# Kernel tuning notes

Hardware: AMD Instinct MI355X
Metric: run time of the kernel (lower is better)

Reference implementation:

```python
import jax, jax.numpy as jnp
import numpy as np

D, H, K = 384, 6, 8

def _ln(x, g, b, eps=1e-5):
    mu = jnp.mean(x, axis=-1, keepdims=True)
    var = jnp.mean((x - mu) ** 2, axis=-1, keepdims=True)
    return (x - mu) * jax.lax.rsqrt(var + eps) * g + b

def setup_inputs() -> dict:
    key = jax.random.key(0)
    ks = jax.random.split(key, 20)
    B, N = 4, 2048
    s = 0.02
    inp = {
        'x': jax.random.normal(ks[0], (B, N, D), jnp.float32),
        'knn_index': jax.random.randint(ks[1], (B * K * N,), 0, B * N, jnp.int64),
        'ln1_g': jnp.ones((D,), jnp.float32),
        'ln1_b': jnp.zeros((D,), jnp.float32),
        'w_qkv': jax.random.normal(ks[2], (D, 3 * D), jnp.float32) * s,
        'w_proj': jax.random.normal(ks[3], (D, D), jnp.float32) * s,
        'b_proj': jnp.zeros((D,), jnp.float32),
        'w_knn': jax.random.normal(ks[4], (2 * D, D), jnp.float32) * s,
        'b_knn': jnp.zeros((D,), jnp.float32),
        'w_g1': jax.random.normal(ks[5], (2 * D, D), jnp.float32) * s,
        'b_g1': jnp.zeros((D,), jnp.float32),
        'w_g2': jax.random.normal(ks[6], (D, D), jnp.float32) * s,
        'b_g2': jnp.zeros((D,), jnp.float32),
        'ln2_g': jnp.ones((D,), jnp.float32),
        'ln2_b': jnp.zeros((D,), jnp.float32),
        'w_fc1': jax.random.normal(ks[7], (D, 4 * D), jnp.float32) * s,
        'b_fc1': jnp.zeros((4 * D,), jnp.float32),
        'w_fc2': jax.random.normal(ks[8], (4 * D, D), jnp.float32) * s,
        'b_fc2': jnp.zeros((D,), jnp.float32),
    }
    return inp

def reference(x, knn_index, ln1_g, ln1_b, w_qkv, w_proj, b_proj, w_knn, b_knn,
              w_g1, b_g1, w_g2, b_g2, ln2_g, ln2_b, w_fc1, b_fc1, w_fc2, b_fc2):
    B, N, _ = x.shape
    hd = D // H
    scale = hd ** -0.5
    nx = _ln(x, ln1_g, ln1_b)
    # --- self attention ---
    qkv = (nx @ w_qkv).reshape(B, N, 3, H, hd).transpose(2, 0, 3, 1, 4)  # [3,B,H,N,hd]
    q, k, v = qkv[0], qkv[1], qkv[2]
    attn = jax.nn.softmax(jnp.einsum('bhnd,bhmd->bhnm', q * scale, k), axis=-1)
    attn_out = jnp.einsum('bhnm,bhmd->bhnd', attn, v).transpose(0, 2, 1, 3).reshape(B, N, D)
    attn_out = attn_out @ w_proj + b_proj
    # --- EdgeConv-style graph feature: gather-concat-MLP-maxpool ---
    feat = nx.reshape(B * N, D)[knn_index].reshape(B, K, N, D)
    xe = jnp.broadcast_to(nx[:, None], (B, K, N, D))
    gf = jnp.concatenate([feat - xe, xe], axis=-1)  # [B,K,N,2D]
    knn_out = jnp.max(jax.nn.leaky_relu(gf @ w_knn + b_knn, 0.2), axis=1)  # [B,N,D]
    # --- salience gate ---
    gi = jnp.concatenate([attn_out, knn_out], axis=-1)
    gate = jax.nn.sigmoid(jax.nn.gelu(gi @ w_g1 + b_g1, approximate=False) @ w_g2 + b_g2)
    fused = (1 - gate) * attn_out + gate * knn_out
    x = x + fused
    # --- FFN ---
    h = jax.nn.gelu(_ln(x, ln2_g, ln2_b) @ w_fc1 + b_fc1, approximate=False)
    x = x + (h @ w_fc2 + b_fc2)
    return x
```

## Files before the change

kernel.cpp:

```cpp
#include <hip/hip_runtime.h>
#include <math.h>

typedef unsigned short u16;
typedef __attribute__((ext_vector_type(8))) short short8;
typedef __attribute__((ext_vector_type(4))) float floatx4;
typedef __attribute__((ext_vector_type(4))) short sh4v;

union sh4u { sh4v v; u16 u[4]; };
union sh8u { short8 v; u16 u[8]; };

__device__ __forceinline__ floatx4 mfma16(short8 a, short8 b, floatx4 c) {
  return __builtin_amdgcn_mfma_f32_16x16x32_bf16(a, b, c, 0, 0, 0);
}

__device__ __forceinline__ floatx4 zero4() {
  floatx4 z = {0.f, 0.f, 0.f, 0.f};
  return z;
}

__device__ __forceinline__ u16 f2b(float f) {
  union { float f; unsigned u; } v; v.f = f;
  unsigned u = v.u;
  return (u16)((u + 0x7FFFu + ((u >> 16) & 1u)) >> 16);
}

__device__ __forceinline__ float b2f(u16 u) {
  union { unsigned u; float f; } v; v.u = ((unsigned)u) << 16;
  return v.f;
}

__device__ __forceinline__ float gelu_exact(float x) {
  return 0.5f * x * (1.f + erff(x * 0.70710678118654752440f));
}

__device__ __forceinline__ unsigned pack2(float a, float b) {
  return (unsigned)f2b(a) | ((unsigned)f2b(b) << 16);
}

__device__ __forceinline__ unsigned permpack(float p0, float p1) {
  return __builtin_amdgcn_perm(__float_as_uint(p1), __float_as_uint(p0), 0x07060302u);
}

__global__ __launch_bounds__(256) void tcln_kernel(
    const float* __restrict__ p0, const float* __restrict__ p1,
    const float* __restrict__ p2, const float* __restrict__ p3,
    const float* __restrict__ p4, const float* __restrict__ p5,
    const float* __restrict__ wknn,
    u16* __restrict__ o0, u16* __restrict__ o1, u16* __restrict__ o2,
    u16* __restrict__ o3, u16* __restrict__ o4, u16* __restrict__ o5,
    u16* __restrict__ wcT,
    const float* __restrict__ x, const float* __restrict__ g,
    const float* __restrict__ bia, u16* __restrict__ nx) {
  __shared__ u16 L[64][66];
  int t = blockIdx.x, tid = threadIdx.x;
  if (t >= 612) {
    int wave = tid >> 6, lane = tid & 63;
    int row = (t - 612) * 4 + wave;
    const float* xr = x + (size_t)row * 384;
    float v[6];
    float s = 0.f;
#pragma unroll
    for (int j = 0; j < 6; j++) { v[j] = xr[lane + 64 * j]; s += v[j]; }
#pragma unroll
    for (int off = 32; off > 0; off >>= 1) s += __shfl_xor(s, off);
    float mu = s * (1.f / 384.f);
    float ss = 0.f;
#pragma unroll
    for (int j = 0; j < 6; j++) { float d = v[j] - mu; ss += d * d; }
#pragma unroll
    for (int off = 32; off > 0; off >>= 1) ss += __shfl_xor(ss, off);
    float rstd = rsqrtf(ss * (1.f / 384.f) + 1e-5f);
    u16* orow = nx + (size_t)row * 384;
#pragma unroll
    for (int j = 0; j < 6; j++) {
      int d = lane + 64 * j;
      orow[d] = f2b((v[j] - mu) * rstd * g[d] + bia[d]);
    }
    return;
  }
  if (t >= 540) {
    t -= 540;
    int tk = t / 12, tn = t % 12;
    int k0 = tk * 64, j0 = tn * 64;
#pragma unroll
    for (int i = 0; i < 4; i++) {
      int c = tid + 256 * i;
      int r = c >> 4, c4 = (c & 15) * 4;
      floatx4 v;
      if (j0 < 384) {
        v = *(const floatx4*)(wknn + (size_t)(k0 + r) * 384 + j0 + c4);
      } else {
        floatx4 a = *(const floatx4*)(wknn + (size_t)(384 + k0 + r) * 384 + (j0 - 384) + c4);
        floatx4 b = *(const floatx4*)(wknn + (size_t)(k0 + r) * 384 + (j0 - 384) + c4);
        v = a - b;
      }
      *(unsigned*)&L[r][c4]     = pack2(v[0], v[1]);
      *(unsigned*)&L[r][c4 + 2] = pack2(v[2], v[3]);
    }
    __syncthreads();
#pragma unroll
    for (int i = 0; i < 2; i++) {
      int c = tid + 256 * i;
      int nn = c >> 3, k8 = (c & 7) * 8;
      sh8u pk;
#pragma unroll
      for (int j = 0; j < 8; j++) pk.u[j] = L[k8 + j][nn];
      *(short8*)(wcT + (size_t)(j0 + nn) * 384 + k0 + k8) = pk.v;
    }
    return;
  }
  const float* src; u16* dst; int Kd, Nd, tk, tn;
  if      (t < 108) { src = p0; dst = o0; Kd = 384;  Nd = 1152; tk = t / 18; tn = t % 18; }
  else if (t < 144) { src = p1; dst = o1; Kd = 384;  Nd = 384;  t -= 108; tk = t / 6;  tn = t % 6; }
  else if (t < 216) { src = p2; dst = o2; Kd = 768;  Nd = 384;  t -= 144; tk = t / 6;  tn = t % 6; }
  else if (t < 252) { src = p3; dst = o3; Kd = 384;  Nd = 384;  t -= 216; tk = t / 6;  tn = t % 6; }
  else if (t < 396) { src = p4; dst = o4; Kd = 384;  Nd = 1536; t -= 252; tk = t / 24; tn = t % 24; }
  else              { src = p5; dst = o5; Kd = 1536; Nd = 384;  t -= 396; tk = t / 6;  tn = t % 6; }
  int k0 = tk * 64, n0 = tn * 64;
#pragma unroll
  for (int i = 0; i < 4; i++) {
    int c = tid + 256 * i;
    int r = c >> 4, c4 = (c & 15) * 4;
    floatx4 v = *(const floatx4*)(src + (size_t)(k0 + r) * Nd + n0 + c4);
    *(unsigned*)&L[r][c4]     = pack2(v[0], v[1]);
    *(unsigned*)&L[r][c4 + 2] = pack2(v[2], v[3]);
  }
  __syncthreads();
#pragma unroll
  for (int i = 0; i < 2; i++) {
    int c = tid + 256 * i;
    int nn = c >> 3, k8 = (c & 7) * 8;
    sh8u pk;
#pragma unroll
    for (int j = 0; j < 8; j++) pk.u[j] = L[k8 + j][nn];
    *(short8*)(dst + (size_t)(n0 + nn) * Kd + k0 + k8) = pk.v;
  }
}

__global__ __launch_bounds__(256) void lnb_kernel(const u16* __restrict__ x,
                                                  const float* __restrict__ g,
                                                  const float* __restrict__ bia,
                                                  u16* __restrict__ out) {
  int wave = threadIdx.x >> 6, lane = threadIdx.x & 63;
  int row = blockIdx.x * 4 + wave;
  const u16* xr = x + (size_t)row * 384;
  float v[6];
  float s = 0.f;
#pragma unroll
  for (int j = 0; j < 6; j++) { v[j] = b2f(xr[lane + 64 * j]); s += v[j]; }
#pragma unroll
  for (int off = 32; off > 0; off >>= 1) s += __shfl_xor(s, off);
  float mu = s * (1.f / 384.f);
  float ss = 0.f;
#pragma unroll
  for (int j = 0; j < 6; j++) { float d = v[j] - mu; ss += d * d; }
#pragma unroll
  for (int off = 32; off > 0; off >>= 1) ss += __shfl_xor(ss, off);
  float rstd = rsqrtf(ss * (1.f / 384.f) + 1e-5f);
  u16* orow = out + (size_t)row * 384;
#pragma unroll
  for (int j = 0; j < 6; j++) {
    int d = lane + 64 * j;
    orow[d] = f2b((v[j] - mu) * rstd * g[d] + bia[d]);
  }
}

template <int EPI>
__global__ __launch_bounds__(256) void gemm128_kernel(
    const u16* __restrict__ A0, const u16* __restrict__ A1, int Ksplit,
    const u16* __restrict__ BwT, const u16* __restrict__ BwT2, int N, int K,
    const float* __restrict__ bias,
    float* __restrict__ outF, u16* __restrict__ outB, u16* __restrict__ outB2,
    const u16* __restrict__ eA16, const u16* __restrict__ eK16,
    const float* __restrict__ eX, u16* __restrict__ outV) {
  __shared__ u16 As[128][72];
  __shared__ u16 Bs[128][72];
  int tid = threadIdx.x;
  int lane = tid & 63, wave = tid >> 6, quad = lane >> 4, l16 = lane & 15;
  int n0 = blockIdx.x * 128, m0 = blockIdx.y * 128;
  int wm = (wave >> 1) * 64, wn = (wave & 1) * 64;
  const u16* Bsrc = BwT;
  int nbase = n0;
  if (EPI == 8 && n0 >= 1152) { Bsrc = BwT2; nbase = n0 - 1152; }
  floatx4 acc[4][4];
#pragma unroll
  for (int i = 0; i < 4; i++)
#pragma unroll
    for (int j = 0; j < 4; j++) acc[i][j] = zero4();

  for (int k0 = 0; k0 < K; k0 += 64) {
    const u16* Ap;
    int kk, sA;
    if (k0 < Ksplit) { Ap = A0; kk = k0; sA = Ksplit; }
    else             { Ap = A1; kk = k0 - Ksplit; sA = K - Ksplit; }
#pragma unroll
    for (int i = 0; i < 4; i++) {
      int c = tid + 256 * i;
      int row = c >> 3, c8 = (c & 7) * 8;
      *(short8*)&As[row][c8] =
          *(const short8*)(Ap + (size_t)(m0 + row) * sA + kk + c8);
      *(short8*)&Bs[row][c8] =
          *(const short8*)(Bsrc + (size_t)(nbase + row) * K + k0 + c8);
    }
    __syncthreads();
#pragma unroll
    for (int kh = 0; kh < 2; kh++) {
      short8 af[4], bfr[4];
#pragma unroll
      for (int ti = 0; ti < 4; ti++)
        af[ti] = *(const short8*)&As[wm + ti * 16 + l16][kh * 32 + quad * 8];
#pragma unroll
      for (int tj = 0; tj < 4; tj++)
        bfr[tj] = *(const short8*)&Bs[wn + tj * 16 + l16][kh * 32 + quad * 8];
#pragma unroll
      for (int ti = 0; ti < 4; ti++)
#pragma unroll
        for (int tj = 0; tj < 4; tj++)
          acc[ti][tj] = mfma16(af[ti], bfr[tj], acc[ti][tj]);
    }
    __syncthreads();
  }

#pragma unroll
  for (int ti = 0; ti < 4; ti++)
#pragma unroll
    for (int tj = 0; tj < 4; tj++) {
      int col = n0 + wn + tj * 16 + l16;
      int row0 = m0 + wm + ti * 16 + quad * 4;
      if (EPI == 8) {
        if (n0 < 1152) {
          float sc = (col < 384) ? 0.18033688011112042f : 1.f;
          sh4u pk;
#pragma unroll
          for (int r = 0; r < 4; r++) {
            u16 bv = f2b(acc[ti][tj][r] * sc);
            outB[(size_t)(row0 + r) * 1152 + col] = bv;
            pk.u[r] = bv;
          }
          if (col >= 768) {
            int b = row0 >> 11, n = row0 & 2047;
            int hd = col - 768;
            *(sh4v*)(outV + ((size_t)(b * 6 + (hd >> 6)) * 64 + (hd & 63)) * 2048 + n) = pk.v;
          }
        } else {
#pragma unroll
          for (int r = 0; r < 4; r++)
            outB2[(size_t)(row0 + r) * 768 + (col - 1152)] = f2b(acc[ti][tj][r]);
        }
      } else {
#pragma unroll
        for (int r = 0; r < 4; r++) {
          size_t rc = (size_t)(row0 + r) * N + col;
          float v = acc[ti][tj][r];
          if (EPI == 3) {
            outB[rc] = f2b(gelu_exact(v + bias[col]));
          } else if (EPI == 4) {
            float gte = 1.f / (1.f + __expf(-(v + bias[col])));
            float fu = (1.f - gte) * b2f(eA16[rc]) + gte * b2f(eK16[rc]);
            outB[rc] = f2b(eX[rc] + fu);
          } else if (EPI == 7) {
            outF[rc] = v + bias[col] + b2f(eA16[rc]);
          }
        }
      }
    }
}

__global__ __launch_bounds__(256) void attn1_kernel(const u16* __restrict__ qkv,
                                                    const u16* __restrict__ Vt,
                                                    u16* __restrict__ OPb,
                                                    float* __restrict__ LS) {
  __shared__ u16 Ks[64][72];
  __shared__ u16 Vts[64][72];
  __shared__ u16 Ps[4][32][72];
  int tid = threadIdx.x;
  int lane = tid & 63, w = tid >> 6, quad = lane >> 4, l16 = lane & 15;
  int bh = blockIdx.y, b = bh / 6, h = bh % 6;
  int q0 = blockIdx.x * 128, split = blockIdx.z;
  const u16* qbase = qkv + (size_t)b * 2048 * 1152 + h * 64;
  const u16* kbase = qbase + 384 + (size_t)split * 512 * 1152;
  const u16* vtb = Vt + (size_t)bh * 64 * 2048 + split * 512;
  short8 qf[2][2];
#pragma unroll
  for (int s = 0; s < 2; s++) {
    int qrow = q0 + w * 32 + s * 16 + l16;
    qf[s][0] = *(const short8*)(qbase + (size_t)qrow * 1152 + quad * 8);
    qf[s][1] = *(const short8*)(qbase + (size_t)qrow * 1152 + 32 + quad * 8);
  }
  floatx4 O[4][2];
  float lsum[2] = {0.f, 0.f};
#pragma unroll
  for (int i = 0; i < 4; i++)
#pragma unroll
    for (int s = 0; s < 2; s++) O[i][s] = zero4();

  int rb = tid >> 3, c8 = (tid & 7) * 8;
  short8 rk[2], rv[2];
  rk[0] = *(const short8*)(kbase + (size_t)rb * 1152 + c8);
  rk[1] = *(const short8*)(kbase + (size_t)(rb + 32) * 1152 + c8);
  rv[0] = *(const short8*)(vtb + (size_t)rb * 2048 + c8);
  rv[1] = *(const short8*)(vtb + (size_t)(rb + 32) * 2048 + c8);

  for (int kt = 0; kt < 8; kt++) {
    __syncthreads();
    *(short8*)&Ks[rb][c8] = rk[0];
    *(short8*)&Ks[rb + 32][c8] = rk[1];
    *(short8*)&Vts[rb][c8] = rv[0];
    *(short8*)&Vts[rb + 32][c8] = rv[1];
    __syncthreads();
    if (kt < 7) {
      int key0 = (kt + 1) * 64;
      rk[0] = *(const short8*)(kbase + (size_t)(key0 + rb) * 1152 + c8);
      rk[1] = *(const short8*)(kbase + (size_t)(key0 + rb + 32) * 1152 + c8);
      rv[0] = *(const short8*)(vtb + (size_t)rb * 2048 + key0 + c8);
      rv[1] = *(const short8*)(vtb + (size_t)(rb + 32) * 2048 + key0 + c8);
    }
#pragma unroll
    for (int mt = 0; mt < 4; mt++) {
      short8 k0 = *(const short8*)&Ks[mt * 16 + l16][quad * 8];
      short8 k1 = *(const short8*)&Ks[mt * 16 + l16][32 + quad * 8];
#pragma unroll
      for (int s = 0; s < 2; s++) {
        floatx4 st = mfma16(k0, qf[s][0], zero4());
        st = mfma16(k1, qf[s][1], st);
        float p0 = exp2f(st[0]), p1 = exp2f(st[1]);
        float p2 = exp2f(st[2]), p3 = exp2f(st[3]);
        lsum[s] += (p0 + p1) + (p2 + p3);
        uint2 pk;
        pk.x = permpack(p0, p1);
        pk.y = permpack(p2, p3);
        *(uint2*)&Ps[w][s * 16 + l16][mt * 16 + quad * 4] = pk;
      }
    }
    short8 pf[2][2];
#pragma unroll
    for (int s = 0; s < 2; s++) {
      pf[s][0] = *(const short8*)&Ps[w][s * 16 + l16][quad * 8];
      pf[s][1] = *(const short8*)&Ps[w][s * 16 + l16][32 + quad * 8];
    }
#pragma unroll
    for (int mt2 = 0; mt2 < 4; mt2++) {
      short8 v0 = *(const short8*)&Vts[mt2 * 16 + l16][quad * 8];
      short8 v1 = *(const short8*)&Vts[mt2 * 16 + l16][32 + quad * 8];
#pragma unroll
      for (int s = 0; s < 2; s++) {
        O[mt2][s] = mfma16(v0, pf[s][0], O[mt2][s]);
        O[mt2][s] = mfma16(v1, pf[s][1], O[mt2][s]);
      }
    }
  }
#pragma unroll
  for (int s = 0; s < 2; s++) {
    lsum[s] += __shfl_xor(lsum[s], 16);
    lsum[s] += __shfl_xor(lsum[s], 32);
    int row = b * 2048 + q0 + w * 32 + s * 16 + l16;
    u16* orow = OPb + (size_t)split * 8192 * 384 + (size_t)row * 384 + h * 64;
#pragma unroll
    for (int mt2 = 0; mt2 < 4; mt2++) {
      sh4u pk;
#pragma unroll
      for (int r = 0; r < 4; r++) pk.u[r] = f2b(O[mt2][s][r]);
      *(sh4v*)(orow + mt2 * 16 + quad * 4) = pk.v;
    }
    if (quad == 0) LS[split * 8192 + row] = lsum[s];
  }
}

__global__ __launch_bounds__(256) void projknn_kernel(
    const u16* __restrict__ OPb, const float* __restrict__ LS,
    const u16* __restrict__ BwT, const float* __restrict__ bias,
    u16* __restrict__ outB,
    const u16* __restrict__ GBb, const int* __restrict__ kidx,
    const float* __restrict__ bknn, u16* __restrict__ knn_bf) {
  __shared__ u16 As[128][72];
  __shared__ u16 Bs[128][72];
  int bid = blockIdx.x, tid = threadIdx.x;
  if (bid >= 192) {
    int wave = tid >> 6, lane = tid & 63;
    int row = (bid - 192) * 4 + wave;
    int b = row >> 11, n = row & 2047;
    float base[6], acc[6];
#pragma unroll
    for (int j = 0; j < 6; j++) {
      int d = lane + 64 * j;
      base[j] = b2f(GBb[(size_t)row * 768 + 384 + d]) + bknn[d];
      acc[j] = -1e30f;
    }
    for (int kk = 0; kk < 8; kk++) {
      int g = kidx[(b * 8 + kk) * 2048 + n];
      const u16* Gr = GBb + (size_t)g * 768;
#pragma unroll
      for (int j = 0; j < 6; j++) {
        float v = b2f(Gr[lane + 64 * j]) + base[j];
        v = v > 0.f ? v : 0.2f * v;
        acc[j] = fmaxf(acc[j], v);
      }
    }
#pragma unroll
    for (int j = 0; j < 6; j++)
      knn_bf[(size_t)row * 384 + lane + 64 * j] = f2b(acc[j]);
    return;
  }
  int lane = tid & 63, wave = tid >> 6, quad = lane >> 4, l16 = lane & 15;
  int n0 = (bid % 3) * 128, m0 = (bid / 3) * 128;
  int wm = (wave >> 1) * 64, wn = (wave & 1) * 64;
  floatx4 acc[4][4];
#pragma unroll
  for (int i = 0; i < 4; i++)
#pragma unroll
    for (int j = 0; j < 4; j++) acc[i][j] = zero4();

  const size_t SP = (size_t)8192 * 384;
  for (int k0 = 0; k0 < 384; k0 += 64) {
#pragma unroll
    for (int i = 0; i < 4; i++) {
      int c = tid + 256 * i;
      int row = c >> 3, c8 = (c & 7) * 8;
      int gr = m0 + row;
      float rl = 1.f / ((LS[gr] + LS[8192 + gr]) + (LS[16384 + gr] + LS[24576 + gr]));
      const u16* p0 = OPb + (size_t)gr * 384 + k0 + c8;
      sh8u a0, a1, a2, a3, pk;
      a0.v = *(const short8*)p0;
      a1.v = *(const short8*)(p0 + SP);
      a2.v = *(const short8*)(p0 + 2 * SP);
      a3.v = *(const short8*)(p0 + 3 * SP);
#pragma unroll
      for (int j = 0; j < 8; j++)
        pk.u[j] = f2b(((b2f(a0.u[j]) + b2f(a1.u[j])) + (b2f(a2.u[j]) + b2f(a3.u[j]))) * rl);
      *(short8*)&As[row][c8] = pk.v;
      *(short8*)&Bs[row][c8] =
          *(const short8*)(BwT + (size_t)(n0 + row) * 384 + k0 + c8);
    }
    __syncthreads();
#pragma unroll
    for (int kh = 0; kh < 2; kh++) {
      short8 af[4], bfr[4];
#pragma unroll
      for (int ti = 0; ti < 4; ti++)
        af[ti] = *(const short8*)&As[wm + ti * 16 + l16][kh * 32 + quad * 8];
#pragma unroll
      for (int tj = 0; tj < 4; tj++)
        bfr[tj] = *(const short8*)&Bs[wn + tj * 16 + l16][kh * 32 + quad * 8];
#pragma unroll
      for (int ti = 0; ti < 4; ti++)
#pragma unroll
        for (int tj = 0; tj < 4; tj++)
          acc[ti][tj] = mfma16(af[ti], bfr[tj], acc[ti][tj]);
    }
    __syncthreads();
  }
#pragma unroll
  for (int ti = 0; ti < 4; ti++)
#pragma unroll
    for (int tj = 0; tj < 4; tj++) {
      int col = n0 + wn + tj * 16 + l16;
      int row0 = m0 + wm + ti * 16 + quad * 4;
#pragma unroll
      for (int r = 0; r < 4; r++)
        outB[(size_t)(row0 + r) * 384 + col] = f2b(acc[ti][tj][r] + bias[col]);
    }
}

extern "C" void kernel_launch(void* const* d_in, const int* in_sizes, int n_in,
                              void* d_out, int out_size, void* d_ws, size_t ws_size,
                              hipStream_t stream) {
  const float* x    = (const float*)d_in[0];
  const int* kidx   = (const int*)d_in[1];
  const float* ln1g = (const float*)d_in[2];
  const float* ln1b = (const float*)d_in[3];
  const float* wqkv = (const float*)d_in[4];
  const float* wproj= (const float*)d_in[5];
  const float* bproj= (const float*)d_in[6];
  const float* wknn = (const float*)d_in[7];
  const float* bknn = (const float*)d_in[8];
  const float* wg1  = (const float*)d_in[9];
  const float* bg1  = (const float*)d_in[10];
  const float* wg2  = (const float*)d_in[11];
  const float* bg2  = (const float*)d_in[12];
  const float* ln2g = (const float*)d_in[13];
  const float* ln2b = (const float*)d_in[14];
  const float* wfc1 = (const float*)d_in[15];
  const float* bfc1 = (const float*)d_in[16];
  const float* wfc2 = (const float*)d_in[17];
  const float* bfc2 = (const float*)d_in[18];
  float* out = (float*)d_out;

  const int M = 8192;
  char* ws = (char*)d_ws;
  size_t off = 0;
  auto alloc = [&](size_t bytes) -> char* {
    char* p = ws + off;
    off += (bytes + 255) & ~(size_t)255;
    return p;
  };
  u16* nx_bf    = (u16*)alloc((size_t)M * 384 * 2);
  u16* qkv_bf   = (u16*)alloc((size_t)M * 1152 * 2);
  u16* attn_bf  = (u16*)alloc((size_t)M * 384 * 2);
  u16* GBb      = (u16*)alloc((size_t)M * 768 * 2);
  u16* knn_bf   = (u16*)alloc((size_t)M * 384 * 2);
  u16* x2b      = (u16*)alloc((size_t)M * 384 * 2);
  u16* t1_bf    = (u16*)alloc((size_t)M * 384 * 2);
  u16* nx2_bf   = (u16*)alloc((size_t)M * 384 * 2);
  u16* Vt_b     = (u16*)alloc((size_t)24 * 64 * 2048 * 2);
  u16* OPb      = (u16*)alloc((size_t)4 * M * 384 * 2);
  float* LS     = (float*)alloc((size_t)4 * M * 4);
  u16* wqkvT    = (u16*)alloc((size_t)1152 * 384 * 2);
  u16* wprojT   = (u16*)alloc(384 * 384 * 2);
  u16* wcT      = (u16*)alloc((size_t)768 * 384 * 2);
  u16* wg1T     = (u16*)alloc((size_t)384 * 768 * 2);
  u16* wg2T     = (u16*)alloc(384 * 384 * 2);
  u16* wfc1T    = (u16*)alloc((size_t)1536 * 384 * 2);
  u16* wfc2T    = (u16*)alloc((size_t)384 * 1536 * 2);
  u16* h_bf     = qkv_bf;

  tcln_kernel<<<2660, 256, 0, stream>>>(wqkv, wproj, wg1, wg2, wfc1, wfc2, wknn,
                                        wqkvT, wprojT, wg1T, wg2T, wfc1T, wfc2T, wcT,
                                        x, ln1g, ln1b, nx_bf);
  gemm128_kernel<8><<<dim3(15, 64), 256, 0, stream>>>(nx_bf, nx_bf, 384, wqkvT, wcT, 1920, 384,
                                                      nullptr, nullptr, qkv_bf, GBb,
                                                      nullptr, nullptr, nullptr, Vt_b);
  attn1_kernel<<<dim3(16, 24, 4), 256, 0, stream>>>(qkv_bf, Vt_b, OPb, LS);
  projknn_kernel<<<2240, 256, 0, stream>>>(OPb, LS, wprojT, bproj, attn_bf,
                                           GBb, kidx, bknn, knn_bf);
  gemm128_kernel<3><<<dim3(3, 64), 256, 0, stream>>>(attn_bf, knn_bf, 384, wg1T, nullptr, 384, 768,
                                                     bg1, nullptr, t1_bf, nullptr,
                                                     nullptr, nullptr, nullptr, nullptr);
  gemm128_kernel<4><<<dim3(3, 64), 256, 0, stream>>>(t1_bf, t1_bf, 384, wg2T, nullptr, 384, 384,
                                                     bg2, nullptr, x2b, nullptr,
                                                     attn_bf, knn_bf, x, nullptr);
  lnb_kernel<<<2048, 256, 0, stream>>>(x2b, ln2g, ln2b, nx2_bf);
  gemm128_kernel<3><<<dim3(12, 64), 256, 0, stream>>>(nx2_bf, nx2_bf, 384, wfc1T, nullptr, 1536, 384,
                                                      bfc1, nullptr, h_bf, nullptr,
                                                      nullptr, nullptr, nullptr, nullptr);
  gemm128_kernel<7><<<dim3(3, 64), 256, 0, stream>>>(h_bf, h_bf, 1536, wfc2T, nullptr, 384, 1536,
                                                     bfc2, out, nullptr, nullptr,
                                                     x2b, nullptr, nullptr, nullptr);
  (void)in_sizes; (void)n_in; (void)out_size; (void)ws_size;
}
```

Measured before the change: 313.7 us.

## Add 64-row prefetching GEMM for narrow outputs and compute attention row sums via MFMA

Adds a gemm64 kernel with 64x128 tiles and register prefetch of the next K tile. It is used for the three N=384 GEMMs (gate1, gate2, fc2), doubling their block count from 192 to 384 to better fill the GPU's compute units. The original gemm128 kernel is simplified by dropping the split-A path and the unused epilogues. In attention, the softmax row sums now come from an MFMA against a vector of bf16 ones instead of scalar adds plus shuffles. This takes VALU work off the exp loop, but sums the bf16-rounded probabilities and adds extra MFMAs.

```diff
diff --git a/kernel.cpp b/kernel.cpp
--- a/kernel.cpp
+++ b/kernel.cpp
@@ -167,12 +167,10 @@
 
 template <int EPI>
 __global__ __launch_bounds__(256) void gemm128_kernel(
-    const u16* __restrict__ A0, const u16* __restrict__ A1, int Ksplit,
-    const u16* __restrict__ BwT, const u16* __restrict__ BwT2, int N, int K,
-    const float* __restrict__ bias,
-    float* __restrict__ outF, u16* __restrict__ outB, u16* __restrict__ outB2,
-    const u16* __restrict__ eA16, const u16* __restrict__ eK16,
-    const float* __restrict__ eX, u16* __restrict__ outV) {
+    const u16* __restrict__ A0, const u16* __restrict__ BwT,
+    const u16* __restrict__ BwT2, int N, int K,
+    const float* __restrict__ bias, u16* __restrict__ outB, u16* __restrict__ outB2,
+    u16* __restrict__ outV) {
   __shared__ u16 As[128][72];
   __shared__ u16 Bs[128][72];
   int tid = threadIdx.x;
@@ -189,16 +187,12 @@
     for (int j = 0; j < 4; j++) acc[i][j] = zero4();
 
   for (int k0 = 0; k0 < K; k0 += 64) {
-    const u16* Ap;
-    int kk, sA;
-    if (k0 < Ksplit) { Ap = A0; kk = k0; sA = Ksplit; }
-    else             { Ap = A1; kk = k0 - Ksplit; sA = K - Ksplit; }
 #pragma unroll
     for (int i = 0; i < 4; i++) {
       int c = tid + 256 * i;
       int row = c >> 3, c8 = (c & 7) * 8;
       *(short8*)&As[row][c8] =
-          *(const short8*)(Ap + (size_t)(m0 + row) * sA + kk + c8);
+          *(const short8*)(A0 + (size_t)(m0 + row) * K + k0 + c8);
       *(short8*)&Bs[row][c8] =
           *(const short8*)(Bsrc + (size_t)(nbase + row) * K + k0 + c8);
     }
@@ -249,18 +243,89 @@
         }
       } else {
 #pragma unroll
-        for (int r = 0; r < 4; r++) {
-          size_t rc = (size_t)(row0 + r) * N + col;
-          float v = acc[ti][tj][r];
-          if (EPI == 3) {
-            outB[rc] = f2b(gelu_exact(v + bias[col]));
-          } else if (EPI == 4) {
-            float gte = 1.f / (1.f + __expf(-(v + bias[col])));
-            float fu = (1.f - gte) * b2f(eA16[rc]) + gte * b2f(eK16[rc]);
-            outB[rc] = f2b(eX[rc] + fu);
-          } else if (EPI == 7) {
-            outF[rc] = v + bias[col] + b2f(eA16[rc]);
-          }
+        for (int r = 0; r < 4; r++)
+          outB[(size_t)(row0 + r) * N + col] = f2b(gelu_exact(acc[ti][tj][r] + bias[col]));
+      }
+    }
+}
+
+template <int EPI>
+__global__ __launch_bounds__(256) void gemm64_kernel(
+    const u16* __restrict__ A0, const u16* __restrict__ A1, int Ksplit,
+    const u16* __restrict__ BwT, int N, int K,
+    const float* __restrict__ bias,
+    float* __restrict__ outF, u16* __restrict__ outB,
+    const u16* __restrict__ eA16, const u16* __restrict__ eK16,
+    const float* __restrict__ eX) {
+  __shared__ u16 As[64][72];
+  __shared__ u16 Bs[128][72];
+  int tid = threadIdx.x;
+  int lane = tid & 63, w = tid >> 6, quad = lane >> 4, l16 = lane & 15;
+  int n0 = blockIdx.x * 128, m0 = blockIdx.y * 64;
+  int ra = tid >> 3, ca = (tid & 7) * 8;
+  floatx4 acc[4][2];
+#pragma unroll
+  for (int i = 0; i < 4; i++)
+#pragma unroll
+    for (int j = 0; j < 2; j++) acc[i][j] = zero4();
+
+  short8 pa[2], pb[4];
+  auto loadAB = [&](int k0) {
+    const u16* Ap;
+    int kk, sA;
+    if (k0 < Ksplit) { Ap = A0; kk = k0; sA = Ksplit; }
+    else             { Ap = A1; kk = k0 - Ksplit; sA = K - Ksplit; }
+    pa[0] = *(const short8*)(Ap + (size_t)(m0 + ra) * sA + kk + ca);
+    pa[1] = *(const short8*)(Ap + (size_t)(m0 + ra + 32) * sA + kk + ca);
+#pragma unroll
+    for (int i = 0; i < 4; i++)
+      pb[i] = *(const short8*)(BwT + (size_t)(n0 + ra + 32 * i) * K + k0 + ca);
+  };
+  loadAB(0);
+  int iters = K >> 6;
+  for (int kt = 0; kt < iters; kt++) {
+    __syncthreads();
+    *(short8*)&As[ra][ca] = pa[0];
+    *(short8*)&As[ra + 32][ca] = pa[1];
+#pragma unroll
+    for (int i = 0; i < 4; i++) *(short8*)&Bs[ra + 32 * i][ca] = pb[i];
+    __syncthreads();
+    if (kt + 1 < iters) loadAB((kt + 1) * 64);
+#pragma unroll
+    for (int kh = 0; kh < 2; kh++) {
+      short8 af[4], bfr[2];
+#pragma unroll
+      for (int mt = 0; mt < 4; mt++)
+        af[mt] = *(const short8*)&As[mt * 16 + l16][kh * 32 + quad * 8];
+#pragma unroll
+      for (int nt = 0; nt < 2; nt++)
+        bfr[nt] = *(const short8*)&Bs[w * 32 + nt * 16 + l16][kh * 32 + quad * 8];
+#pragma unroll
+      for (int mt = 0; mt < 4; mt++)
+#pragma unroll
+        for (int nt = 0; nt < 2; nt++)
+          acc[mt][nt] = mfma16(af[mt], bfr[nt], acc[mt][nt]);
+    }
+  }
+
+#pragma unroll
+  for (int mt = 0; mt < 4; mt++)
+#pragma unroll
+    for (int nt = 0; nt < 2; nt++) {
+      int col = n0 + w * 32 + nt * 16 + l16;
+      int row0 = m0 + mt * 16 + quad * 4;
+#pragma unroll
+      for (int r = 0; r < 4; r++) {
+        size_t rc = (size_t)(row0 + r) * N + col;
+        float v = acc[mt][nt][r];
+        if (EPI == 3) {
+          outB[rc] = f2b(gelu_exact(v + bias[col]));
+        } else if (EPI == 4) {
+          float gte = 1.f / (1.f + __expf(-(v + bias[col])));
+          float fu = (1.f - gte) * b2f(eA16[rc]) + gte * b2f(eK16[rc]);
+          outB[rc] = f2b(eX[rc] + fu);
+        } else if (EPI == 7) {
+          outF[rc] = v + bias[col] + b2f(eA16[rc]);
         }
       }
     }
@@ -287,8 +352,11 @@
     qf[s][0] = *(const short8*)(qbase + (size_t)qrow * 1152 + quad * 8);
     qf[s][1] = *(const short8*)(qbase + (size_t)qrow * 1152 + 32 + quad * 8);
   }
+  short8 ones;
+#pragma unroll
+  for (int j = 0; j < 8; j++) ones[j] = (short)0x3F80;
   floatx4 O[4][2];
-  float lsum[2] = {0.f, 0.f};
+  floatx4 accL[2] = {zero4(), zero4()};
 #pragma unroll
   for (int i = 0; i < 4; i++)
 #pragma unroll
@@ -323,12 +391,9 @@
       for (int s = 0; s < 2; s++) {
         floatx4 st = mfma16(k0, qf[s][0], zero4());
         st = mfma16(k1, qf[s][1], st);
-        float p0 = exp2f(st[0]), p1 = exp2f(st[1]);
-        float p2 = exp2f(st[2]), p3 = exp2f(st[3]);
-        lsum[s] += (p0 + p1) + (p2 + p3);
         uint2 pk;
-        pk.x = permpack(p0, p1);
-        pk.y = permpack(p2, p3);
+        pk.x = permpack(exp2f(st[0]), exp2f(st[1]));
+        pk.y = permpack(exp2f(st[2]), exp2f(st[3]));
         *(uint2*)&Ps[w][s * 16 + l16][mt * 16 + quad * 4] = pk;
       }
     }
@@ -337,6 +402,8 @@
     for (int s = 0; s < 2; s++) {
       pf[s][0] = *(const short8*)&Ps[w][s * 16 + l16][quad * 8];
       pf[s][1] = *(const short8*)&Ps[w][s * 16 + l16][32 + quad * 8];
+      accL[s] = mfma16(ones, pf[s][0], accL[s]);
+      accL[s] = mfma16(ones, pf[s][1], accL[s]);
     }
 #pragma unroll
     for (int mt2 = 0; mt2 < 4; mt2++) {
@@ -351,8 +418,6 @@
   }
 #pragma unroll
   for (int s = 0; s < 2; s++) {
-    lsum[s] += __shfl_xor(lsum[s], 16);
-    lsum[s] += __shfl_xor(lsum[s], 32);
     int row = b * 2048 + q0 + w * 32 + s * 16 + l16;
     u16* orow = OPb + (size_t)split * 8192 * 384 + (size_t)row * 384 + h * 64;
 #pragma unroll
@@ -362,7 +427,7 @@
       for (int r = 0; r < 4; r++) pk.u[r] = f2b(O[mt2][s][r]);
       *(sh4v*)(orow + mt2 * 16 + quad * 4) = pk.v;
     }
-    if (quad == 0) LS[split * 8192 + row] = lsum[s];
+    if (quad == 0) LS[split * 8192 + row] = accL[s][0];
   }
 }
 
@@ -516,24 +581,22 @@
   tcln_kernel<<<2660, 256, 0, stream>>>(wqkv, wproj, wg1, wg2, wfc1, wfc2, wknn,
                                         wqkvT, wprojT, wg1T, wg2T, wfc1T, wfc2T, wcT,
                                         x, ln1g, ln1b, nx_bf);
-  gemm128_kernel<8><<<dim3(15, 64), 256, 0, stream>>>(nx_bf, nx_bf, 384, wqkvT, wcT, 1920, 384,
-                                                      nullptr, nullptr, qkv_bf, GBb,
-                                                      nullptr, nullptr, nullptr, Vt_b);
+  gemm128_kernel<8><<<dim3(15, 64), 256, 0, stream>>>(nx_bf, wqkvT, wcT, 1920, 384,
+                                                      nullptr, qkv_bf, GBb, Vt_b);
   attn1_kernel<<<dim3(16, 24, 4), 256, 0, stream>>>(qkv_bf, Vt_b, OPb, LS);
   projknn_kernel<<<2240, 256, 0, stream>>>(OPb, LS, wprojT, bproj, attn_bf,
                                            GBb, kidx, bknn, knn_bf);
-  gemm128_kernel<3><<<dim3(3, 64), 256, 0, stream>>>(attn_bf, knn_bf, 384, wg1T, nullptr, 384, 768,
-                                                     bg1, nullptr, t1_bf, nullptr,
-                                                     nullptr, nullptr, nullptr, nullptr);
-  gemm128_kernel<4><<<dim3(3, 64), 256, 0, stream>>>(t1_bf, t1_bf, 384, wg2T, nullptr, 384, 384,
-                                                     bg2, nullptr, x2b, nullptr,
-                                                     attn_bf, knn_bf, x, nullptr);
+  gemm64_kernel<3><<<dim3(3, 128), 256, 0, stream>>>(attn_bf, knn_bf, 384, wg1T, 384, 768,
+                                                     bg1, nullptr, t1_bf,
+                                                     nullptr, nullptr, nullptr);
+  gemm64_kernel<4><<<dim3(3, 128), 256, 0, stream>>>(t1_bf, t1_bf, 384, wg2T, 384, 384,
+                                                     bg2, nullptr, x2b,
+                                                     attn_bf, knn_bf, x);
   lnb_kernel<<<2048, 256, 0, stream>>>(x2b, ln2g, ln2b, nx2_bf);
-  gemm128_kernel<3><<<dim3(12, 64), 256, 0, stream>>>(nx2_bf, nx2_bf, 384, wfc1T, nullptr, 1536, 384,
-                                                      bfc1, nullptr, h_bf, nullptr,
-                                                      nullptr, nullptr, nullptr, nullptr);
-  gemm128_kernel<7><<<dim3(3, 64), 256, 0, stream>>>(h_bf, h_bf, 1536, wfc2T, nullptr, 384, 1536,
-                                                     bfc2, out, nullptr, nullptr,
-                                                     x2b, nullptr, nullptr, nullptr);
+  gemm128_kernel<3><<<dim3(12, 64), 256, 0, stream>>>(nx2_bf, wfc1T, nullptr, 1536, 384,
+                                                      bfc1, h_bf, nullptr, nullptr);
+  gemm64_kernel<7><<<dim3(3, 128), 256, 0, stream>>>(h_bf, h_bf, 1536, wfc2T, 384, 1536,
+                                                     bfc2, out, nullptr,
+                                                     x2b, nullptr, nullptr);
   (void)in_sizes; (void)n_in; (void)out_size; (void)ws_size;
 }
```

Result: faster. 297.8 us (-5.1%).
